# Optimization experiments

Measured on AMD Instinct MI355X. Metric: run time of the kernel, lower is better.

The kernel has to match this reference:

```python
import jax, jax.numpy as jnp
import numpy as np

B, C = 262144, 14  # batch, num_labels (CheXpert 14 labels)
MAX_T = C - 1      # max_num_trials
L_PARAM = 14       # self.l
KAPPA = 2.0
RAMP_CAP = 1.8     # 1 - s with s = -0.8


def setup_inputs() -> dict:
    key = jax.random.key(0)
    k1, k2, k3, k4 = jax.random.split(key, 4)
    inp = jax.random.normal(k1, (B, C), dtype=jnp.float32)
    target = jax.random.randint(k2, (B, C), 0, 2, dtype=jnp.int32)
    S = jax.random.uniform(k3, (B,), dtype=jnp.float32)
    # pre-drawn uniforms driving the sequential negative-sampling trials
    rand_u = jax.random.uniform(k4, (B, C, MAX_T), dtype=jnp.float32)
    return {"inp": inp, "target": target, "S": S, "rand_u": rand_u}


def reference(inp, target, S, rand_u):
    # L[i] = sum_{r=1..i+1} 1/r  (harmonic weights), indices 0..L_PARAM-1
    L = jnp.cumsum(1.0 / (jnp.arange(L_PARAM, dtype=inp.dtype) + 1.0))

    neg_mask = target == 0                      # [B,C]
    pos_mask = target == 1                      # [B,C]
    num_neg = neg_mask.sum(axis=1)              # [B]

    # negative label positions packed to the front of each row (stable)
    order = jnp.argsort(jnp.where(neg_mask, 0, 1), axis=1, stable=True)  # [B,C]

    rows = jnp.arange(B)[:, None, None]
    # uniform choice among the num_neg negatives, per (i, j, trial)
    t_idx = jnp.clip((rand_u * num_neg[:, None, None].astype(rand_u.dtype)).astype(jnp.int32),
                     0, jnp.maximum(num_neg - 1, 0)[:, None, None])       # [B,C,T]
    neg_sample = order[rows, t_idx]                                       # [B,C,T]

    # sequential trial loop: stop at first margin >= 0, cap at MAX_T trials
    margins = 1.0 - inp[:, :, None] + inp[rows, neg_sample]               # [B,C,T]
    nonneg = margins >= 0
    first = jnp.argmax(nonneg, axis=2)                                    # 0 if none
    num_trials = jnp.where(nonneg.any(axis=2), first + 1, MAX_T)          # [B,C]
    r_j = MAX_T // num_trials                                             # floor
    weight = L[r_j]                                                       # [B,C]

    # ramp(1 - inp[i,j] + inp[i,k]) = clip(inp[i,j] - inp[i,k], 0, 1.8)
    pairwise = jnp.clip(inp[:, :, None] - inp[:, None, :], 0.0, RAMP_CAP)  # [B,C(j),C(k)]
    neg_sum = jnp.sum(pairwise * neg_mask[:, None, :].astype(inp.dtype), axis=2)  # [B,C]

    # s_i = 1 for i <= l, else S[i - l]
    idx = jnp.arange(B)
    s_i = jnp.where(idx <= L_PARAM, 1.0, S[jnp.maximum(idx - L_PARAM, 0)])  # [B]

    valid = pos_mask & (num_neg > 0)[:, None]  # skip positives with no negatives
    loss_warp = jnp.sum(s_i[:, None] * jnp.where(valid, weight * neg_sum, 0.0))

    # kappa term: ramp(target * inp) over all labels
    ramp_k = jnp.clip(1.0 - target.astype(inp.dtype) * inp, 0.0, RAMP_CAP)
    loss_kappa = KAPPA * jnp.sum(s_i[:, None] * ramp_k)

    return loss_warp + loss_kappa
```

## Files before the change

kernel.cpp:

```cpp
#include <hip/hip_runtime.h>

#define CC   14
#define MAXT 13
#define TPB  256
#define RAMP_CAP 1.8f

constexpr float H2  = 1.0f + 0.5f;
constexpr float H3  = H2  + (1.0f/3.0f);
constexpr float H4  = H3  + 0.25f;
constexpr float H5  = H4  + 0.2f;
constexpr float H6  = H5  + (1.0f/6.0f);
constexpr float H7  = H6  + (1.0f/7.0f);
constexpr float H14 = H7 + 0.125f + (1.0f/9.0f) + 0.1f + (1.0f/11.0f)
                         + (1.0f/12.0f) + (1.0f/13.0f) + (1.0f/14.0f);

template<int PAR, int J>
__device__ __forceinline__ void do_label(unsigned pm, int nn, float fnn,
                                         const float* __restrict__ rowF,
                                         const float (&x)[CC], float& lw)
{
    if ((pm >> J) & 1u) {
        constexpr int SH = (J + 2 * PAR) & 3;
        const float* qp = rowF + (13 * J - SH);
        float4 q0 = *(const float4*)(qp);
        float4 q1 = *(const float4*)(qp + 4);
        float4 q2 = *(const float4*)(qp + 8);
        const float e[12] = {q0.x,q0.y,q0.z,q0.w, q1.x,q1.y,q1.z,q1.w,
                             q2.x,q2.y,q2.z,q2.w};

        const float m1 = 1.0f - x[J];
        float nsum = 0.f; unsigned gm = 0; int cnt = 0;
        #pragma unroll
        for (int k = 0; k < CC; ++k) {
            if (!((pm >> k) & 1u)) {
                nsum += fminf(fmaxf(x[J] - x[k], 0.f), RAMP_CAP);
                if (m1 + x[k] >= 0.f) gm |= (1u << cnt);
                ++cnt;
            }
        }

        unsigned bits = 0;
        #pragma unroll
        for (int t = 0; t < 8; ++t) {
            int ti = (int)(e[SH + t] * fnn);
            ti = ti < 0 ? 0 : ti;
            ti = ti > nn - 1 ? nn - 1 : ti;
            bits |= ((gm >> ti) & 1u) << t;
        }
        if (bits == 0u) {
            #pragma unroll
            for (int t = 8; t < MAXT; ++t) {
                int ti = (int)(rowF[13 * J + t] * fnn);
                ti = ti < 0 ? 0 : ti;
                ti = ti > nn - 1 ? nn - 1 : ti;
                bits |= ((gm >> ti) & 1u) << t;
            }
        }
        const int nt = bits ? __ffs(bits) : MAXT;
        const float wt = (nt == 1) ? H14 : (nt == 2) ? H7
                       : (nt == 3) ? H5  : (nt == 4) ? H4
                       : (nt <= 6) ? H3  : H2;
        lw += wt * nsum;
    }
}

template<int PAR>
__device__ __forceinline__ float row_contrib(int row,
    const float* __restrict__ inp, const int* __restrict__ target,
    const float* __restrict__ S, const float* __restrict__ rand_u)
{
    float x[CC];
    {
        const float* b = inp + (size_t)row * CC;
        if constexpr (PAR == 0) {
            float4 a0 = *(const float4*)(b);
            float4 a1 = *(const float4*)(b + 4);
            float4 a2 = *(const float4*)(b + 8);
            float2 a3 = *(const float2*)(b + 12);
            x[0]=a0.x; x[1]=a0.y; x[2]=a0.z; x[3]=a0.w;
            x[4]=a1.x; x[5]=a1.y; x[6]=a1.z; x[7]=a1.w;
            x[8]=a2.x; x[9]=a2.y; x[10]=a2.z; x[11]=a2.w;
            x[12]=a3.x; x[13]=a3.y;
        } else {
            float2 a0 = *(const float2*)(b);
            float4 a1 = *(const float4*)(b + 2);
            float4 a2 = *(const float4*)(b + 6);
            float4 a3 = *(const float4*)(b + 10);
            x[0]=a0.x; x[1]=a0.y;
            x[2]=a1.x; x[3]=a1.y; x[4]=a1.z; x[5]=a1.w;
            x[6]=a2.x; x[7]=a2.y; x[8]=a2.z; x[9]=a2.w;
            x[10]=a3.x; x[11]=a3.y; x[12]=a3.z; x[13]=a3.w;
        }
    }
    int tg[CC];
    {
        const int* b = target + (size_t)row * CC;
        if constexpr (PAR == 0) {
            int4 a0 = *(const int4*)(b);
            int4 a1 = *(const int4*)(b + 4);
            int4 a2 = *(const int4*)(b + 8);
            int2 a3 = *(const int2*)(b + 12);
            tg[0]=a0.x; tg[1]=a0.y; tg[2]=a0.z; tg[3]=a0.w;
            tg[4]=a1.x; tg[5]=a1.y; tg[6]=a1.z; tg[7]=a1.w;
            tg[8]=a2.x; tg[9]=a2.y; tg[10]=a2.z; tg[11]=a2.w;
            tg[12]=a3.x; tg[13]=a3.y;
        } else {
            int2 a0 = *(const int2*)(b);
            int4 a1 = *(const int4*)(b + 2);
            int4 a2 = *(const int4*)(b + 6);
            int4 a3 = *(const int4*)(b + 10);
            tg[0]=a0.x; tg[1]=a0.y;
            tg[2]=a1.x; tg[3]=a1.y; tg[4]=a1.z; tg[5]=a1.w;
            tg[6]=a2.x; tg[7]=a2.y; tg[8]=a2.z; tg[9]=a2.w;
            tg[10]=a3.x; tg[11]=a3.y; tg[12]=a3.z; tg[13]=a3.w;
        }
    }

    unsigned pm = 0; float kap = 0.f;
    #pragma unroll
    for (int k = 0; k < CC; ++k) {
        if (tg[k] != 0) {
            pm |= (1u << k);
            kap += fminf(fmaxf(1.0f - x[k], 0.f), RAMP_CAP);
        } else {
            kap += 1.0f;
        }
    }
    const int nn = CC - __popc(pm);

    float lw = 0.f;
    if (pm != 0u && nn > 0) {
        const float fnn = (float)nn;
        const float* rowF = rand_u + (size_t)row * (CC * MAXT);
        do_label<PAR, 0>(pm, nn, fnn, rowF, x, lw);
        do_label<PAR, 1>(pm, nn, fnn, rowF, x, lw);
        do_label<PAR, 2>(pm, nn, fnn, rowF, x, lw);
        do_label<PAR, 3>(pm, nn, fnn, rowF, x, lw);
        do_label<PAR, 4>(pm, nn, fnn, rowF, x, lw);
        do_label<PAR, 5>(pm, nn, fnn, rowF, x, lw);
        do_label<PAR, 6>(pm, nn, fnn, rowF, x, lw);
        do_label<PAR, 7>(pm, nn, fnn, rowF, x, lw);
        do_label<PAR, 8>(pm, nn, fnn, rowF, x, lw);
        do_label<PAR, 9>(pm, nn, fnn, rowF, x, lw);
        do_label<PAR,10>(pm, nn, fnn, rowF, x, lw);
        do_label<PAR,11>(pm, nn, fnn, rowF, x, lw);
        do_label<PAR,12>(pm, nn, fnn, rowF, x, lw);
        do_label<PAR,13>(pm, nn, fnn, rowF, x, lw);
    }
    const float si = (row <= 14) ? 1.0f : S[row - 14];
    return si * (lw + 2.0f * kap);
}

__global__ __launch_bounds__(TPB) void rwl_kernel(
    const float* __restrict__ inp, const int* __restrict__ target,
    const float* __restrict__ S, const float* __restrict__ rand_u,
    float* __restrict__ out, int B)
{
    __shared__ float s_red[4];
    const int tid  = threadIdx.x;
    const int pair = blockIdx.x * TPB + tid;
    const int r0 = pair * 2, r1 = r0 + 1;

    float total = 0.f;
    if (r0 < B) total += row_contrib<0>(r0, inp, target, S, rand_u);
    if (r1 < B) total += row_contrib<1>(r1, inp, target, S, rand_u);

    #pragma unroll
    for (int off = 32; off > 0; off >>= 1)
        total += __shfl_down(total, off, 64);
    const int wave = tid >> 6;
    if ((tid & 63) == 0) s_red[wave] = total;
    __syncthreads();
    if (tid == 0)
        atomicAdd(out, s_red[0] + s_red[1] + s_red[2] + s_red[3]);
}

extern "C" void kernel_launch(void* const* d_in, const int* in_sizes, int n_in,
                              void* d_out, int out_size, void* d_ws, size_t ws_size,
                              hipStream_t stream) {
    const float* inp    = (const float*)d_in[0];
    const int*   target = (const int*)d_in[1];
    const float* S      = (const float*)d_in[2];
    const float* ru     = (const float*)d_in[3];
    float*       out    = (float*)d_out;
    const int B = in_sizes[2];

    hipMemsetAsync(out, 0, sizeof(float), stream);

    const int pairs  = (B + 1) / 2;
    const int blocks = (pairs + TPB - 1) / TPB;
    rwl_kernel<<<blocks, TPB, 0, stream>>>(inp, target, S, ru, out, B);
}
```

Measured before the change: 51.13 us.

## Split each row pair's labels across four waves and shrink speculative prefetch

Each block now covers 64 row pairs, and the label loop for each row is divided among four wavefronts (labels j mod 4), with wave 0 also computing the kappa term. This spreads the per-row serial label work over four times as many threads, so there is more parallelism and less per-thread latency. Each wave still reloads the row's inputs and targets, which adds redundant load instructions, although those hit in cache. The speculative vector prefetch of rand_u is cut from 12 to 8 floats, and only the first 4 trials are checked eagerly, so rows that need more trials go through the slower scalar fallback path more often.

```diff
diff --git a/kernel.cpp b/kernel.cpp
--- a/kernel.cpp
+++ b/kernel.cpp
@@ -24,9 +24,7 @@
         const float* qp = rowF + (13 * J - SH);
         float4 q0 = *(const float4*)(qp);
         float4 q1 = *(const float4*)(qp + 4);
-        float4 q2 = *(const float4*)(qp + 8);
-        const float e[12] = {q0.x,q0.y,q0.z,q0.w, q1.x,q1.y,q1.z,q1.w,
-                             q2.x,q2.y,q2.z,q2.w};
+        const float e[8] = {q0.x,q0.y,q0.z,q0.w, q1.x,q1.y,q1.z,q1.w};
 
         const float m1 = 1.0f - x[J];
         float nsum = 0.f; unsigned gm = 0; int cnt = 0;
@@ -41,7 +39,7 @@
 
         unsigned bits = 0;
         #pragma unroll
-        for (int t = 0; t < 8; ++t) {
+        for (int t = 0; t < 4; ++t) {
             int ti = (int)(e[SH + t] * fnn);
             ti = ti < 0 ? 0 : ti;
             ti = ti > nn - 1 ? nn - 1 : ti;
@@ -49,7 +47,7 @@
         }
         if (bits == 0u) {
             #pragma unroll
-            for (int t = 8; t < MAXT; ++t) {
+            for (int t = 4; t < MAXT; ++t) {
                 int ti = (int)(rowF[13 * J + t] * fnn);
                 ti = ti < 0 ? 0 : ti;
                 ti = ti > nn - 1 ? nn - 1 : ti;
@@ -65,7 +63,7 @@
 }
 
 template<int PAR>
-__device__ __forceinline__ float row_contrib(int row,
+__device__ __forceinline__ float row_part(int row, int c,
     const float* __restrict__ inp, const int* __restrict__ target,
     const float* __restrict__ S, const float* __restrict__ rand_u)
 {
@@ -92,9 +90,10 @@
             x[10]=a3.x; x[11]=a3.y; x[12]=a3.z; x[13]=a3.w;
         }
     }
-    int tg[CC];
+    unsigned pm = 0;
     {
         const int* b = target + (size_t)row * CC;
+        int tg[CC];
         if constexpr (PAR == 0) {
             int4 a0 = *(const int4*)(b);
             int4 a1 = *(const int4*)(b + 4);
@@ -114,17 +113,8 @@
             tg[6]=a2.x; tg[7]=a2.y; tg[8]=a2.z; tg[9]=a2.w;
             tg[10]=a3.x; tg[11]=a3.y; tg[12]=a3.z; tg[13]=a3.w;
         }
-    }
-
-    unsigned pm = 0; float kap = 0.f;
-    #pragma unroll
-    for (int k = 0; k < CC; ++k) {
-        if (tg[k] != 0) {
-            pm |= (1u << k);
-            kap += fminf(fmaxf(1.0f - x[k], 0.f), RAMP_CAP);
-        } else {
-            kap += 1.0f;
-        }
+        #pragma unroll
+        for (int k = 0; k < CC; ++k) if (tg[k] != 0) pm |= (1u << k);
     }
     const int nn = CC - __popc(pm);
 
@@ -132,23 +122,44 @@
     if (pm != 0u && nn > 0) {
         const float fnn = (float)nn;
         const float* rowF = rand_u + (size_t)row * (CC * MAXT);
-        do_label<PAR, 0>(pm, nn, fnn, rowF, x, lw);
-        do_label<PAR, 1>(pm, nn, fnn, rowF, x, lw);
-        do_label<PAR, 2>(pm, nn, fnn, rowF, x, lw);
-        do_label<PAR, 3>(pm, nn, fnn, rowF, x, lw);
-        do_label<PAR, 4>(pm, nn, fnn, rowF, x, lw);
-        do_label<PAR, 5>(pm, nn, fnn, rowF, x, lw);
-        do_label<PAR, 6>(pm, nn, fnn, rowF, x, lw);
-        do_label<PAR, 7>(pm, nn, fnn, rowF, x, lw);
-        do_label<PAR, 8>(pm, nn, fnn, rowF, x, lw);
-        do_label<PAR, 9>(pm, nn, fnn, rowF, x, lw);
-        do_label<PAR,10>(pm, nn, fnn, rowF, x, lw);
-        do_label<PAR,11>(pm, nn, fnn, rowF, x, lw);
-        do_label<PAR,12>(pm, nn, fnn, rowF, x, lw);
-        do_label<PAR,13>(pm, nn, fnn, rowF, x, lw);
+        switch (c) {
+        case 0:
+            do_label<PAR, 0>(pm, nn, fnn, rowF, x, lw);
+            do_label<PAR, 4>(pm, nn, fnn, rowF, x, lw);
+            do_label<PAR, 8>(pm, nn, fnn, rowF, x, lw);
+            do_label<PAR,12>(pm, nn, fnn, rowF, x, lw);
+            break;
+        case 1:
+            do_label<PAR, 1>(pm, nn, fnn, rowF, x, lw);
+            do_label<PAR, 5>(pm, nn, fnn, rowF, x, lw);
+            do_label<PAR, 9>(pm, nn, fnn, rowF, x, lw);
+            do_label<PAR,13>(pm, nn, fnn, rowF, x, lw);
+            break;
+        case 2:
+            do_label<PAR, 2>(pm, nn, fnn, rowF, x, lw);
+            do_label<PAR, 6>(pm, nn, fnn, rowF, x, lw);
+            do_label<PAR,10>(pm, nn, fnn, rowF, x, lw);
+            break;
+        default:
+            do_label<PAR, 3>(pm, nn, fnn, rowF, x, lw);
+            do_label<PAR, 7>(pm, nn, fnn, rowF, x, lw);
+            do_label<PAR,11>(pm, nn, fnn, rowF, x, lw);
+            break;
+        }
+    }
+
+    float v = lw;
+    if (c == 0) {
+        float kap = 0.f;
+        #pragma unroll
+        for (int k = 0; k < CC; ++k) {
+            if ((pm >> k) & 1u) kap += fminf(fmaxf(1.0f - x[k], 0.f), RAMP_CAP);
+            else                kap += 1.0f;
+        }
+        v += 2.0f * kap;
     }
     const float si = (row <= 14) ? 1.0f : S[row - 14];
-    return si * (lw + 2.0f * kap);
+    return si * v;
 }
 
 __global__ __launch_bounds__(TPB) void rwl_kernel(
@@ -158,18 +169,18 @@
 {
     __shared__ float s_red[4];
     const int tid  = threadIdx.x;
-    const int pair = blockIdx.x * TPB + tid;
-    const int r0 = pair * 2, r1 = r0 + 1;
+    const int p = blockIdx.x * 64 + (tid & 63);
+    const int c = __builtin_amdgcn_readfirstlane(tid >> 6);
+    const int r0 = p * 2, r1 = r0 + 1;
 
     float total = 0.f;
-    if (r0 < B) total += row_contrib<0>(r0, inp, target, S, rand_u);
-    if (r1 < B) total += row_contrib<1>(r1, inp, target, S, rand_u);
+    if (r0 < B) total += row_part<0>(r0, c, inp, target, S, rand_u);
+    if (r1 < B) total += row_part<1>(r1, c, inp, target, S, rand_u);
 
     #pragma unroll
     for (int off = 32; off > 0; off >>= 1)
         total += __shfl_down(total, off, 64);
-    const int wave = tid >> 6;
-    if ((tid & 63) == 0) s_red[wave] = total;
+    if ((tid & 63) == 0) s_red[tid >> 6] = total;
     __syncthreads();
     if (tid == 0)
         atomicAdd(out, s_red[0] + s_red[1] + s_red[2] + s_red[3]);
@@ -188,6 +199,6 @@
     hipMemsetAsync(out, 0, sizeof(float), stream);
 
     const int pairs  = (B + 1) / 2;
-    const int blocks = (pairs + TPB - 1) / TPB;
+    const int blocks = (pairs + 63) / 64;
     rwl_kernel<<<blocks, TPB, 0, stream>>>(inp, target, S, ru, out, B);
 }
```

Measured after the change: 64.37 us. 25.9% more time.

## Assign one row per thread with wave-uniform parity and trim speculative rand_u loads

Applied to the files above, without the earlier changes.

Each thread now processes a single row instead of two. Rows are interleaved so that each wave holds rows of one parity, which keeps the template specialisation wave-uniform via readfirstlane and doubles the number of threads launched. The speculative prefetch of uniforms per positive label drops from 12 to 4–8 floats and the initial check covers 4 trials instead of 8. The fallback loop is skipped when no negative can yield a nonnegative margin. Together these aim to raise memory-level parallelism and cut wasted rand_u traffic. The cost is more scattered scalar loads whenever the first 4 trials all fail.

```diff
diff --git a/kernel.cpp b/kernel.cpp
--- a/kernel.cpp
+++ b/kernel.cpp
@@ -22,11 +22,15 @@
     if ((pm >> J) & 1u) {
         constexpr int SH = (J + 2 * PAR) & 3;
         const float* qp = rowF + (13 * J - SH);
-        float4 q0 = *(const float4*)(qp);
-        float4 q1 = *(const float4*)(qp + 4);
-        float4 q2 = *(const float4*)(qp + 8);
-        const float e[12] = {q0.x,q0.y,q0.z,q0.w, q1.x,q1.y,q1.z,q1.w,
-                             q2.x,q2.y,q2.z,q2.w};
+        float e[8];
+        {
+            float4 q0 = *(const float4*)(qp);
+            e[0]=q0.x; e[1]=q0.y; e[2]=q0.z; e[3]=q0.w;
+        }
+        if constexpr (SH != 0) {
+            float4 q1 = *(const float4*)(qp + 4);
+            e[4]=q1.x; e[5]=q1.y; e[6]=q1.z; e[7]=q1.w;
+        }
 
         const float m1 = 1.0f - x[J];
         float nsum = 0.f; unsigned gm = 0; int cnt = 0;
@@ -41,15 +45,15 @@
 
         unsigned bits = 0;
         #pragma unroll
-        for (int t = 0; t < 8; ++t) {
+        for (int t = 0; t < 4; ++t) {
             int ti = (int)(e[SH + t] * fnn);
             ti = ti < 0 ? 0 : ti;
             ti = ti > nn - 1 ? nn - 1 : ti;
             bits |= ((gm >> ti) & 1u) << t;
         }
-        if (bits == 0u) {
+        if (bits == 0u && gm != 0u) {
             #pragma unroll
-            for (int t = 8; t < MAXT; ++t) {
+            for (int t = 4; t < MAXT; ++t) {
                 int ti = (int)(rowF[13 * J + t] * fnn);
                 ti = ti < 0 ? 0 : ti;
                 ti = ti > nn - 1 ? nn - 1 : ti;
@@ -92,9 +96,10 @@
             x[10]=a3.x; x[11]=a3.y; x[12]=a3.z; x[13]=a3.w;
         }
     }
-    int tg[CC];
+    unsigned pm = 0; float kap = 0.f;
     {
         const int* b = target + (size_t)row * CC;
+        int tg[CC];
         if constexpr (PAR == 0) {
             int4 a0 = *(const int4*)(b);
             int4 a1 = *(const int4*)(b + 4);
@@ -114,16 +119,14 @@
             tg[6]=a2.x; tg[7]=a2.y; tg[8]=a2.z; tg[9]=a2.w;
             tg[10]=a3.x; tg[11]=a3.y; tg[12]=a3.z; tg[13]=a3.w;
         }
-    }
-
-    unsigned pm = 0; float kap = 0.f;
-    #pragma unroll
-    for (int k = 0; k < CC; ++k) {
-        if (tg[k] != 0) {
-            pm |= (1u << k);
-            kap += fminf(fmaxf(1.0f - x[k], 0.f), RAMP_CAP);
-        } else {
-            kap += 1.0f;
+        #pragma unroll
+        for (int k = 0; k < CC; ++k) {
+            if (tg[k] != 0) {
+                pm |= (1u << k);
+                kap += fminf(fmaxf(1.0f - x[k], 0.f), RAMP_CAP);
+            } else {
+                kap += 1.0f;
+            }
         }
     }
     const int nn = CC - __popc(pm);
@@ -151,25 +154,28 @@
     return si * (lw + 2.0f * kap);
 }
 
-__global__ __launch_bounds__(TPB) void rwl_kernel(
+__global__ __launch_bounds__(TPB, 4) void rwl_kernel(
     const float* __restrict__ inp, const int* __restrict__ target,
     const float* __restrict__ S, const float* __restrict__ rand_u,
     float* __restrict__ out, int B)
 {
     __shared__ float s_red[4];
     const int tid  = threadIdx.x;
-    const int pair = blockIdx.x * TPB + tid;
-    const int r0 = pair * 2, r1 = r0 + 1;
+    const int lane = tid & 63;
+    const int wid  = tid >> 6;
+    const int row = blockIdx.x * TPB + ((wid >> 1) << 7) + (lane << 1) + (wid & 1);
+    const int par = __builtin_amdgcn_readfirstlane(wid & 1);
 
     float total = 0.f;
-    if (r0 < B) total += row_contrib<0>(r0, inp, target, S, rand_u);
-    if (r1 < B) total += row_contrib<1>(r1, inp, target, S, rand_u);
+    if (row < B) {
+        if (par == 0) total = row_contrib<0>(row, inp, target, S, rand_u);
+        else          total = row_contrib<1>(row, inp, target, S, rand_u);
+    }
 
     #pragma unroll
     for (int off = 32; off > 0; off >>= 1)
         total += __shfl_down(total, off, 64);
-    const int wave = tid >> 6;
-    if ((tid & 63) == 0) s_red[wave] = total;
+    if ((tid & 63) == 0) s_red[wid] = total;
     __syncthreads();
     if (tid == 0)
         atomicAdd(out, s_red[0] + s_red[1] + s_red[2] + s_red[3]);
@@ -187,7 +193,6 @@
 
     hipMemsetAsync(out, 0, sizeof(float), stream);
 
-    const int pairs  = (B + 1) / 2;
-    const int blocks = (pairs + TPB - 1) / TPB;
+    const int blocks = (B + TPB - 1) / TPB;
     rwl_kernel<<<blocks, TPB, 0, stream>>>(inp, target, S, ru, out, B);
 }
```

Result: faster. 47.80 us (-6.5%).
